# Kernel optimization log

Measured on AMD Instinct MI355X. Metric: run time of the kernel, lower is better.

## Reference

```python
import jax, jax.numpy as jnp
import numpy as np

EPS_NORM = 1e-6
EPS_MM = 1e-5


def feature_l2norm(f, axis=1):
    # torch: f / sqrt(sum(f^2, dim) + 1e-6)
    return f / jnp.sqrt(jnp.sum(f * f, axis=axis, keepdims=True) + EPS_NORM)


def mutual_matching(c):
    # c: [b, 1, f1, f2, f3, f4]
    b, ch, f1, f2, f3, f4 = c.shape
    # max over (f1,f2) for each (f3,f4) target location
    max_B = jnp.max(c.reshape(b, f1 * f2, f3, f4), axis=1).reshape(b, 1, 1, 1, f3, f4)
    # max over (f3,f4) for each (f1,f2) source location
    max_A = jnp.max(c.reshape(b, f1 * f2, f3 * f4), axis=2).reshape(b, 1, f1, f2, 1, 1)
    return c * (c / (max_A + EPS_MM)) * (c / (max_B + EPS_MM))


def correlation4d(fa, fb):
    # fa: [b,c,hA,wA], fb: [b,c,hB,wB] -> [b,1,hA,wA,hB,wB]
    corr = jnp.einsum('bcij,bckl->bijkl', fa, fb)[:, None]
    corr = jax.nn.relu(corr)
    return feature_l2norm(corr, axis=1)  # channel dim is 1 -> x/sqrt(x^2+eps)


def conv4d(x, w, b):
    # x: [B,Ci,f1,f2,f3,f4]; w: [Co,Ci,k,k,k,k]; b: [Co]
    # Implemented as a sum of k 3D convs over (f2,f3,f4), sliding along f1 --
    # exactly the Conv4d emulation used by NC-Net.
    B, Ci, f1, f2, f3, f4 = x.shape
    Co, _, k = w.shape[:3]
    p = k // 2
    xp = jnp.pad(x, ((0, 0), (0, 0), (p, p), (0, 0), (0, 0), (0, 0)))
    out = None
    for i in range(k):
        xi = jax.lax.dynamic_slice_in_dim(xp, i, f1, axis=2)        # [B,Ci,f1,f2,f3,f4]
        xi = xi.transpose(0, 2, 1, 3, 4, 5).reshape(B * f1, Ci, f2, f3, f4)
        yi = jax.lax.conv_general_dilated(
            xi, w[:, :, i], window_strides=(1, 1, 1),
            padding=[(p, p)] * 3,
            dimension_numbers=('NCDHW', 'OIDHW', 'NCDHW'))
        yi = yi.reshape(B, f1, Co, f2, f3, f4).transpose(0, 2, 1, 3, 4, 5)
        out = yi if out is None else out + yi
    return out + b[None, :, None, None, None, None]


def nc_stack(x, params):
    # Sequential(Conv4d, ReLU) x 3
    for w, b in params:
        x = jax.nn.relu(conv4d(x, w, b))
    return x


def neigh_consensus(x, params):
    # symmetric mode: conv(x) + conv(x.permute(0,1,4,5,2,3)).permute back
    ya = nc_stack(x, params)
    yb = nc_stack(x.transpose(0, 1, 4, 5, 2, 3), params).transpose(0, 1, 4, 5, 2, 3)
    return ya + yb


def setup_inputs() -> dict:
    key = jax.random.key(0)
    ks = jax.random.split(key, 8)
    b, c, h, w = 4, 256, 32, 32
    feature_A = jax.random.normal(ks[0], (b, c, h, w), dtype=jnp.float32)
    feature_B = jax.random.normal(ks[1], (b, c, h, w), dtype=jnp.float32)
    k = 3
    w1 = jax.random.normal(ks[2], (10, 1, k, k, k, k), dtype=jnp.float32) * 0.05
    b1 = jnp.zeros((10,), jnp.float32)
    w2 = jax.random.normal(ks[3], (10, 10, k, k, k, k), dtype=jnp.float32) * 0.05
    b2 = jnp.zeros((10,), jnp.float32)
    w3 = jax.random.normal(ks[4], (1, 10, k, k, k, k), dtype=jnp.float32) * 0.05
    b3 = jnp.zeros((1,), jnp.float32)
    return {"feature_A": feature_A, "feature_B": feature_B,
            "w1": w1, "b1": b1, "w2": w2, "b2": b2, "w3": w3, "b3": b3}


def reference(feature_A, feature_B, w1, b1, w2, b2, w3, b3):
    fa = feature_l2norm(feature_A, axis=1)
    fb = feature_l2norm(feature_B, axis=1)
    corr4d = correlation4d(fa, fb)                   # [b,1,hA,wA,hB,wB]
    corr4d = mutual_matching(corr4d)
    corr4d = neigh_consensus(corr4d, [(w1, b1), (w2, b2), (w3, b3)])
    corr4d = mutual_matching(corr4d)
    return corr4d
```

## Files before the change

kernel.cpp:

```cpp
#include <hip/hip_runtime.h>

#define EPSN 1e-6f
#define EPSM 1e-5f

typedef __fp16 h2v __attribute__((ext_vector_type(2)));
typedef __fp16 f16x4 __attribute__((ext_vector_type(4)));
typedef float f32x4 __attribute__((ext_vector_type(4)));

#define MFMA16(a, b, c) __builtin_amdgcn_mfma_f32_16x16x16f16((a), (b), (c), 0, 0, 0)

__device__ __forceinline__ unsigned pkh2(float a, float b) {
    union { h2v h; unsigned u; } v;
    v.h = __builtin_amdgcn_cvt_pkrtz(a, b);
    return v.u;
}

__device__ __forceinline__ float dot2f(unsigned a, unsigned b, float c) {
    union { unsigned u; h2v h; } ua, ub;
    ua.u = a; ub.u = b;
#if __has_builtin(__builtin_amdgcn_fdot2)
    return __builtin_amdgcn_fdot2(ua.h, ub.h, c, false);
#else
    return fmaf((float)ua.h.x, (float)ub.h.x,
                fmaf((float)ua.h.y, (float)ub.h.y, c));
#endif
}

__global__ __launch_bounds__(256) void invnorm_k(const float* __restrict__ f,
                                                 float* __restrict__ inv)
{
    int pbase = blockIdx.x * 64;
    int pp = threadIdx.x & 63;
    int cc = threadIdx.x >> 6;
    int pos = pbase + pp;
    int b = pos >> 10, ij = pos & 1023;
    const float* fp = f + (size_t)(b * 256) * 1024 + ij;
    float s = 0.f;
    #pragma unroll 8
    for (int k = 0; k < 64; ++k) {
        float v = fp[(size_t)(cc * 64 + k) * 1024];
        s += v * v;
    }
    __shared__ float red[4][64];
    red[cc][pp] = s;
    __syncthreads();
    if (cc == 0) {
        float t = red[0][pp] + red[1][pp] + red[2][pp] + red[3][pp];
        inv[pos] = rsqrtf(t + EPSN);
    }
}

__global__ __launch_bounds__(256) void corr_k(const float* __restrict__ fa,
                                              const float* __restrict__ fb,
                                              const float* __restrict__ invA,
                                              const float* __restrict__ invB,
                                              float* __restrict__ corr)
{
    __shared__ float As[16][68];
    __shared__ float Bs[16][68];
    int b = blockIdx.z;
    int i0 = blockIdx.y * 64, j0 = blockIdx.x * 64;
    int tid = threadIdx.x;
    int tx = tid & 15, ty = tid >> 4;
    const float* fab = fa + (size_t)b * 256 * 1024;
    const float* fbb = fb + (size_t)b * 256 * 1024;
    const float* ia = invA + b * 1024 + i0;
    const float* ib = invB + b * 1024 + j0;
    float acc[4][4] = {};
    for (int kc = 0; kc < 256; kc += 16) {
        #pragma unroll
        for (int l = 0; l < 4; ++l) {
            int idx = tid + l * 256;
            int r = idx >> 6, cix = idx & 63;
            As[r][cix] = fab[(size_t)(kc + r) * 1024 + i0 + cix] * ia[cix];
            Bs[r][cix] = fbb[(size_t)(kc + r) * 1024 + j0 + cix] * ib[cix];
        }
        __syncthreads();
        #pragma unroll
        for (int k = 0; k < 16; ++k) {
            float4 av = *(const float4*)&As[k][ty * 4];
            float4 bv = *(const float4*)&Bs[k][tx * 4];
            float a[4] = {av.x, av.y, av.z, av.w};
            float bq[4] = {bv.x, bv.y, bv.z, bv.w};
            #pragma unroll
            for (int ii = 0; ii < 4; ++ii)
                #pragma unroll
                for (int jj = 0; jj < 4; ++jj)
                    acc[ii][jj] += a[ii] * bq[jj];
        }
        __syncthreads();
    }
    float* cb = corr + ((size_t)b << 20);
    #pragma unroll
    for (int ii = 0; ii < 4; ++ii) {
        float4 o; float v;
        v = fmaxf(acc[ii][0], 0.f); o.x = v * rsqrtf(v * v + EPSN);
        v = fmaxf(acc[ii][1], 0.f); o.y = v * rsqrtf(v * v + EPSN);
        v = fmaxf(acc[ii][2], 0.f); o.z = v * rsqrtf(v * v + EPSN);
        v = fmaxf(acc[ii][3], 0.f); o.w = v * rsqrtf(v * v + EPSN);
        *(float4*)&cb[(size_t)(i0 + ty * 4 + ii) * 1024 + j0 + tx * 4] = o;
    }
}

__global__ __launch_bounds__(256) void rowmax_k(const float* __restrict__ c,
                                                float* __restrict__ maxR)
{
    int b = blockIdx.y, i = blockIdx.x, tid = threadIdx.x;
    const float* row = c + ((size_t)b << 20) + ((size_t)i << 10);
    float m = fmaxf(fmaxf(row[tid], row[tid + 256]), fmaxf(row[tid + 512], row[tid + 768]));
    #pragma unroll
    for (int off = 32; off; off >>= 1) m = fmaxf(m, __shfl_down(m, off, 64));
    __shared__ float sred[4];
    if ((tid & 63) == 0) sred[tid >> 6] = m;
    __syncthreads();
    if (tid == 0)
        maxR[b * 1024 + i] = fmaxf(fmaxf(sred[0], sred[1]), fmaxf(sred[2], sred[3]));
}

__global__ __launch_bounds__(256) void colmax_k(const float* __restrict__ c,
                                                float* __restrict__ maxC)
{
    int j = blockIdx.x * 256 + threadIdx.x;
    int r0 = blockIdx.y * 128;
    int b = blockIdx.z;
    const float* cb = c + ((size_t)b << 20);
    float m = 0.f;
    for (int r = 0; r < 128; ++r) m = fmaxf(m, cb[(size_t)(r0 + r) * 1024 + j]);
    atomicMax((int*)&maxC[b * 1024 + j], __float_as_int(m));
}

__global__ __launch_bounds__(256) void mmapply_k(float* __restrict__ c,
                                                 const float* __restrict__ maxR,
                                                 const float* __restrict__ maxC)
{
    int e4 = blockIdx.x * 256 + threadIdx.x;
    int e = e4 * 4;
    int b = e >> 20, i = (e >> 10) & 1023, j0 = e & 1023;
    float4 v = ((float4*)c)[e4];
    float ra = 1.f / (maxR[b * 1024 + i] + EPSM);
    float4 mb = ((const float4*)maxC)[(b * 1024 + j0) >> 2];
    float4 o;
    o.x = v.x * v.x * v.x * ra / (mb.x + EPSM);
    o.y = v.y * v.y * v.y * ra / (mb.y + EPSM);
    o.z = v.z * v.z * v.z * ra / (mb.z + EPSM);
    o.w = v.w * v.w * v.w * ra / (mb.w + EPSM);
    ((float4*)c)[e4] = o;
}

template <int CI, int CO>
__global__ void packw_k(const float* __restrict__ w, float* __restrict__ dst, int perm)
{
    constexpr int WS = (3 * CO + 3) & ~3;
    int idx = blockIdx.x * 256 + threadIdx.x;
    if (idx >= CI * 27 * WS) return;
    int ci = idx / (27 * WS);
    int rem = idx - ci * 27 * WS;
    int d123 = rem / WS;
    int slot = rem - d123 * WS;
    float v = 0.f;
    if (slot < 3 * CO) {
        int d4 = slot / CO, co = slot - d4 * CO;
        int t = d123 * 3 + d4;
        int d1 = t / 27, r2 = t % 27;
        int d2 = r2 / 9, r3 = r2 % 9;
        int d3 = r3 / 3, dd4 = r3 % 3;
        int st = perm ? (d3 * 27 + dd4 * 9 + d1 * 3 + d2) : t;
        v = w[(co * CI + ci) * 81 + st];
    }
    dst[idx] = v;
}

__global__ void packwm_k(const float* __restrict__ w, unsigned short* __restrict__ dst,
                         int perm)
{
    int idx = blockIdx.x * 256 + threadIdx.x;
    if (idx >= 20736) return;
    int tap = idx >> 8;
    int co  = (idx >> 4) & 15;
    int k   = idx & 15;
    float v = 0.f;
    if (co < 10 && k < 10) {
        int d1 = tap / 27, r2 = tap % 27;
        int d2 = r2 / 9, r3 = r2 % 9;
        int d3 = r3 / 3, d4 = r3 % 3;
        int st = perm ? (d3 * 27 + d4 * 9 + d1 * 3 + d2) : tap;
        v = w[(co * 10 + k) * 81 + st];
    }
    union { __fp16 h; unsigned short u; } cv;
    cv.h = (__fp16)v;
    dst[idx] = cv.u;
}

template <int CIP, int CO>
__global__ void packw2_k(const float* __restrict__ w, unsigned* __restrict__ dst, int perm)
{
    constexpr int WS = (3 * CO + 3) & ~3;
    int idx = blockIdx.x * 256 + threadIdx.x;
    if (idx >= CIP * 27 * WS) return;
    int pp = idx / (27 * WS);
    int rem = idx - pp * 27 * WS;
    int d123 = rem / WS;
    int slot = rem - d123 * WS;
    unsigned v = 0u;
    if (slot < 3 * CO) {
        int d4 = slot / CO, co = slot - d4 * CO;
        int t = d123 * 3 + d4;
        int d1 = t / 27, r2 = t % 27;
        int d2 = r2 / 9, r3 = r2 % 9;
        int d3 = r3 / 3, dd4 = r3 % 3;
        int st = perm ? (d3 * 27 + dd4 * 9 + d1 * 3 + d2) : t;
        float f0 = w[(co * 2 * CIP + 2 * pp) * 81 + st];
        float f1 = w[(co * 2 * CIP + 2 * pp + 1) * 81 + st];
        v = pkh2(f0, f1);
    }
    dst[idx] = v;
}

template <int CI, int CO, bool ADD, bool PACK>
__global__ __launch_bounds__(256, 4) void conv4d_k(const float* __restrict__ x,
                                                   const float* __restrict__ wp,
                                                   const float* __restrict__ bias,
                                                   float* __restrict__ y)
{
    constexpr int WS = (3 * CO + 3) & ~3;
    constexpr int NW4 = WS / 4;
    constexpr int SLAB = 34 * 35;
    __shared__ float tile[3 * SLAB];

    int tid = threadIdx.x;
    int f1 = blockIdx.x >> 5, f2 = blockIdx.x & 31;
    int q = tid & 7, yy = tid >> 3;
    int x0 = q << 2;

    for (int e = tid; e < 3 * SLAB; e += 256) tile[e] = 0.f;

    float acc[CO][4];
    #pragma unroll
    for (int co = 0; co < CO; ++co) {
        float bv = bias[co];
        acc[co][0] = bv; acc[co][1] = bv; acc[co][2] = bv; acc[co][3] = bv;
    }

    float bufA[WS], bufB[WS];

#define TAP(U, WB, WN, PF) do {                                               \
        constexpr int u_ = (U);                                               \
        const float* rowb_ = &tile[(u_/3)*SLAB + (yy + u_%3)*35 + x0];        \
        float xs_[6];                                                         \
        _Pragma("unroll") for (int j = 0; j < 6; ++j) xs_[j] = rowb_[j];      \
        if (PF) {                                                             \
            _Pragma("unroll") for (int k = 0; k < NW4; ++k)                   \
                *(float4*)&WN[k*4] =                                          \
                    ((const float4*)(wphase + (u_+1)*WS))[k];                 \
        }                                                                     \
        _Pragma("unroll") for (int d4 = 0; d4 < 3; ++d4)                      \
        _Pragma("unroll") for (int co = 0; co < CO; ++co) {                   \
            float wf_ = WB[d4*CO + co];                                       \
            _Pragma("unroll") for (int p = 0; p < 4; ++p)                     \
                acc[co][p] = fmaf(xs_[p + d4], wf_, acc[co][p]);              \
        }                                                                     \
    } while (0)

    #pragma unroll 1
    for (int ci = 0; ci < CI; ++ci) {
        const float* wci = wp + ci * 27 * WS;
        #pragma unroll 1
        for (int d1 = 0; d1 < 3; ++d1) {
            int g1 = f1 + d1 - 1;
            bool g1ok = (unsigned)g1 < 32u;
            const float* wphase = wci + d1 * 9 * WS;
            __syncthreads();
            #pragma unroll
            for (int k = 0; k < NW4; ++k)
                *(float4*)&bufA[k*4] = ((const float4*)wphase)[k];
            #pragma unroll
            for (int it = 0; it < 3; ++it) {
                int e = tid + it * 256;
                int s2 = e >> 8, rr = (e >> 3) & 31, qq = e & 7;
                int g2 = f2 + s2 - 1;
                float4 v = {0.f, 0.f, 0.f, 0.f};
                if (g1ok & ((unsigned)g2 < 32u))
                    v = *(const float4*)&x[((size_t)ci << 20) +
                        ((size_t)((g1 << 5) + g2) << 10) + (rr << 5) + (qq << 2)];
                float* t = &tile[s2 * SLAB + (rr + 1) * 35 + 1 + (qq << 2)];
                t[0] = v.x; t[1] = v.y; t[2] = v.z; t[3] = v.w;
            }
            __syncthreads();

            TAP(0, bufA, bufB, true);
            TAP(1, bufB, bufA, true);
            TAP(2, bufA, bufB, true);
            TAP(3, bufB, bufA, true);
            TAP(4, bufA, bufB, true);
            TAP(5, bufB, bufA, true);
            TAP(6, bufA, bufB, true);
            TAP(7, bufB, bufA, true);
            TAP(8, bufA, bufB, false);
        }
    }
#undef TAP

    size_t obase = ((size_t)(f1 * 32 + f2) << 10) + yy * 32 + x0;
    if (PACK) {
        unsigned* ypu = (unsigned*)y;
        #pragma unroll
        for (int c = 0; c < CO / 2; ++c) {
            uint4 o;
            o.x = pkh2(fmaxf(acc[2*c][0], 0.f), fmaxf(acc[2*c+1][0], 0.f));
            o.y = pkh2(fmaxf(acc[2*c][1], 0.f), fmaxf(acc[2*c+1][1], 0.f));
            o.z = pkh2(fmaxf(acc[2*c][2], 0.f), fmaxf(acc[2*c+1][2], 0.f));
            o.w = pkh2(fmaxf(acc[2*c][3], 0.f), fmaxf(acc[2*c+1][3], 0.f));
            *(uint4*)&ypu[(size_t)c * 1048576 + obase] = o;
        }
    } else {
        #pragma unroll
        for (int co = 0; co < CO; ++co) {
            float4 o;
            o.x = fmaxf(acc[co][0], 0.f);
            o.y = fmaxf(acc[co][1], 0.f);
            o.z = fmaxf(acc[co][2], 0.f);
            o.w = fmaxf(acc[co][3], 0.f);
            float* yp = y + ((size_t)co << 20) + obase;
            if (ADD) {
                float4 prev = *(const float4*)yp;
                o.x += prev.x; o.y += prev.y; o.z += prev.z; o.w += prev.w;
            }
            *(float4*)yp = o;
        }
    }
}

__global__ __launch_bounds__(256, 4) void conv4dm_k(const unsigned* __restrict__ xp,
                                                    const unsigned short* __restrict__ wm,
                                                    const float* __restrict__ bias,
                                                    unsigned* __restrict__ yp)
{
    __shared__ unsigned tile[3 * 10 * 34 * 9];

    int tid = threadIdx.x;
    int bx = blockIdx.x;
    int chunk  = bx & 7;
    int within = bx >> 3;
    int f1 = (chunk << 2) | (within >> 7);
    int f2 = (within >> 2) & 31;
    int q  = within & 3;

    int l  = tid & 63;
    int wv = tid >> 6;
    int sl = l & 15;
    int g  = l >> 4;

    for (int e = tid; e < 9180; e += 256) tile[e] = 0u;

    f32x4 bv;
    #pragma unroll
    for (int e = 0; e < 4; ++e) {
        int co = 4 * g + e;
        bv[e] = (co < 10) ? bias[co] : 0.f;
    }
    f32x4 acc0 = bv, acc1 = bv, acc2 = bv, acc3 = bv;

    int qbase = q * 8;

    #pragma unroll 1
    for (int d1 = 0; d1 < 3; ++d1) {
        int g1 = f1 + d1 - 1;
        bool g1ok = (unsigned)g1 < 32u;
        __syncthreads();

        uint2 aw[27];
        #pragma unroll
        for (int t27 = 0; t27 < 27; ++t27) {
            int tap = d1 * 27 + t27;
            aw[t27] = *(const uint2*)&wm[(tap << 8) + (sl << 4) + (g << 2)];
        }

        if (tid < 240) {
            int k  = tid & 7;
            int rg = tid >> 3;
            int r  = rg % 10;
            int s2 = rg / 10;
            int c  = 1 + (k << 2);
            int g2 = f2 + s2 - 1;
            int g3 = qbase + r - 1;
            uint4 v0 = {0,0,0,0}, v1 = {0,0,0,0}, v2 = {0,0,0,0},
                  v3 = {0,0,0,0}, v4 = {0,0,0,0};
            if (g1ok & ((unsigned)g2 < 32u) & ((unsigned)g3 < 32u)) {
                size_t off = ((size_t)((g1 << 5) + g2) << 10) + (g3 << 5) + (c - 1);
                v0 = *(const uint4*)&xp[off];
                v1 = *(const uint4*)&xp[off + 1048576];
                v2 = *(const uint4*)&xp[off + 2097152];
                v3 = *(const uint4*)&xp[off + 3145728];
                v4 = *(const uint4*)&xp[off + 4194304];
            }
            unsigned* tb = &tile[((s2 * 10 + r) * 34 + c) * 9];
            tb[0] = v0.x; tb[9]  = v0.y; tb[18] = v0.z; tb[27] = v0.w;
            tb[1] = v1.x; tb[10] = v1.y; tb[19] = v1.z; tb[28] = v1.w;
            tb[2] = v2.x; tb[11] = v2.y; tb[20] = v2.z; tb[29] = v2.w;
            tb[3] = v3.x; tb[12] = v3.y; tb[21] = v3.z; tb[30] = v3.w;
            tb[4] = v4.x; tb[13] = v4.y; tb[22] = v4.z; tb[31] = v4.w;
        }
        __syncthreads();

        int tb0 = ((wv * 2 + 0) * 34 + sl) * 9 + (g << 1);
        #pragma unroll
        for (int d2 = 0; d2 < 3; ++d2)
        #pragma unroll
        for (int d3 = 0; d3 < 3; ++d3)
        #pragma unroll
        for (int d4 = 0; d4 < 3; ++d4) {
            int t27 = d2 * 9 + d3 * 3 + d4;
            union { uint2 u; f16x4 h; } A; A.u = aw[t27];
            int tapoff = ((d2 * 10 + d3) * 34 + d4) * 9;
            const unsigned* bp = &tile[tb0 + tapoff];
            union { uint2 u; f16x4 h; } B;
            B.u.x = bp[0];           B.u.y = bp[1];
            acc0 = MFMA16(A.h, B.h, acc0);
            B.u.x = bp[16 * 9];      B.u.y = bp[16 * 9 + 1];
            acc1 = MFMA16(A.h, B.h, acc1);
            B.u.x = bp[34 * 9];      B.u.y = bp[34 * 9 + 1];
            acc2 = MFMA16(A.h, B.h, acc2);
            B.u.x = bp[50 * 9];      B.u.y = bp[50 * 9 + 1];
            acc3 = MFMA16(A.h, B.h, acc3);
        }
    }

    __syncthreads();
#define EPST(ACC, RT, CH) do {                                                \
        int row_ = (RT);                                                      \
        int col_ = (CH) * 16 + sl;                                            \
        float r0 = fmaxf((ACC)[0], 0.f), r1 = fmaxf((ACC)[1], 0.f);           \
        float r2 = fmaxf((ACC)[2], 0.f), r3 = fmaxf((ACC)[3], 0.f);           \
        if (g < 2) {                                                          \
            tile[((2*g)     * 8 + row_) * 33 + col_] = pkh2(r0, r1);          \
            tile[((2*g + 1) * 8 + row_) * 33 + col_] = pkh2(r2, r3);          \
        } else if (g == 2) {                                                  \
            tile[(4 * 8 + row_) * 33 + col_] = pkh2(r0, r1);                  \
        }                                                                     \
    } while (0)
    EPST(acc0, wv * 2 + 0, 0);
    EPST(acc1, wv * 2 + 0, 1);
    EPST(acc2, wv * 2 + 1, 0);
    EPST(acc3, wv * 2 + 1, 1);
#undef EPST
    __syncthreads();

    size_t pbase = ((size_t)((f1 << 5) + f2) << 10);
    #pragma unroll
    for (int u = tid; u < 320; u += 256) {
        int p   = u >> 6;
        int rem = u & 63;
        int row = rem >> 3;
        int cg  = rem & 7;
        const unsigned* src = &tile[(p * 8 + row) * 33 + (cg << 2)];
        uint4 v;
        v.x = src[0]; v.y = src[1]; v.z = src[2]; v.w = src[3];
        *(uint4*)&yp[(size_t)p * 1048576 + pbase +
                     ((size_t)(qbase + row) << 5) + (cg << 2)] = v;
    }
}

template <int CIP, int CO, bool ADD>
__global__ __launch_bounds__(256, 4) void conv4dp_k(const unsigned* __restrict__ xp,
                                                    const unsigned* __restrict__ wp,
                                                    const float* __restrict__ bias,
                                                    float* __restrict__ y)
{
    constexpr int WS = (3 * CO + 3) & ~3;
    constexpr int NW4 = WS / 4;
    constexpr int SLAB = 34 * 35;
    __shared__ unsigned tile[3 * SLAB];

    int tid = threadIdx.x;
    int f1 = blockIdx.x >> 5, f2 = blockIdx.x & 31;
    int q = tid & 7, yy = tid >> 3;
    int x0 = q << 2;

    for (int e = tid; e < 3 * SLAB; e += 256) tile[e] = 0u;

    float acc[CO][4];
    #pragma unroll
    for (int co = 0; co < CO; ++co) {
        float bvv = bias[co];
        acc[co][0] = bvv; acc[co][1] = bvv; acc[co][2] = bvv; acc[co][3] = bvv;
    }

    unsigned bufA[WS], bufB[WS];

#define TAPP(U, WB, WN, PF) do {                                              \
        constexpr int u_ = (U);                                               \
        const unsigned* rowb_ = &tile[(u_/3)*SLAB + (yy + u_%3)*35 + x0];     \
        unsigned xs_[6];                                                      \
        _Pragma("unroll") for (int j = 0; j < 6; ++j) xs_[j] = rowb_[j];      \
        if (PF) {                                                             \
            _Pragma("unroll") for (int k = 0; k < NW4; ++k)                   \
                *(uint4*)&WN[k*4] =                                           \
                    ((const uint4*)(wphase + (u_+1)*WS))[k];                  \
        }                                                                     \
        _Pragma("unroll") for (int d4 = 0; d4 < 3; ++d4)                      \
        _Pragma("unroll") for (int co = 0; co < CO; ++co) {                   \
            unsigned wf_ = WB[d4*CO + co];                                    \
            _Pragma("unroll") for (int p = 0; p < 4; ++p)                     \
                acc[co][p] = dot2f(xs_[p + d4], wf_, acc[co][p]);             \
        }                                                                     \
    } while (0)

    #pragma unroll 1
    for (int pp = 0; pp < CIP; ++pp) {
        const unsigned* wci = wp + pp * 27 * WS;
        #pragma unroll 1
        for (int d1 = 0; d1 < 3; ++d1) {
            int g1 = f1 + d1 - 1;
            bool g1ok = (unsigned)g1 < 32u;
            const unsigned* wphase = wci + d1 * 9 * WS;
            __syncthreads();
            #pragma unroll
            for (int k = 0; k < NW4; ++k)
                *(uint4*)&bufA[k*4] = ((const uint4*)wphase)[k];
            #pragma unroll
            for (int it = 0; it < 3; ++it) {
                int e = tid + it * 256;
                int s2 = e >> 8, rr = (e >> 3) & 31, qq = e & 7;
                int g2 = f2 + s2 - 1;
                uint4 v = {0u, 0u, 0u, 0u};
                if (g1ok & ((unsigned)g2 < 32u))
                    v = *(const uint4*)&xp[((size_t)pp << 20) +
                        ((size_t)((g1 << 5) + g2) << 10) + (rr << 5) + (qq << 2)];
                unsigned* t = &tile[s2 * SLAB + (rr + 1) * 35 + 1 + (qq << 2)];
                t[0] = v.x; t[1] = v.y; t[2] = v.z; t[3] = v.w;
            }
            __syncthreads();

            TAPP(0, bufA, bufB, true);
            TAPP(1, bufB, bufA, true);
            TAPP(2, bufA, bufB, true);
            TAPP(3, bufB, bufA, true);
            TAPP(4, bufA, bufB, true);
            TAPP(5, bufB, bufA, true);
            TAPP(6, bufA, bufB, true);
            TAPP(7, bufB, bufA, true);
            TAPP(8, bufA, bufB, false);
        }
    }
#undef TAPP

    size_t obase = ((size_t)(f1 * 32 + f2) << 10) + yy * 32 + x0;
    #pragma unroll
    for (int co = 0; co < CO; ++co) {
        float4 o;
        o.x = fmaxf(acc[co][0], 0.f);
        o.y = fmaxf(acc[co][1], 0.f);
        o.z = fmaxf(acc[co][2], 0.f);
        o.w = fmaxf(acc[co][3], 0.f);
        float* ypt = y + ((size_t)co << 20) + obase;
        if (ADD) {
            float4 prev = *(const float4*)ypt;
            o.x += prev.x; o.y += prev.y; o.z += prev.z; o.w += prev.w;
        }
        *(float4*)ypt = o;
    }
}

extern "C" void kernel_launch(void* const* d_in, const int* in_sizes, int n_in,
                              void* d_out, int out_size, void* d_ws, size_t ws_size,
                              hipStream_t stream)
{
    (void)in_sizes; (void)n_in; (void)out_size; (void)ws_size;
    const float* fA = (const float*)d_in[0];
    const float* fB = (const float*)d_in[1];
    const float* w1 = (const float*)d_in[2];
    const float* b1 = (const float*)d_in[3];
    const float* w2 = (const float*)d_in[4];
    const float* b2 = (const float*)d_in[5];
    const float* w3 = (const float*)d_in[6];
    const float* b3 = (const float*)d_in[7];
    float* out = (float*)d_out;
    float* ws = (float*)d_ws;

    size_t o = 0;
    float* invA = ws + o; o += 4096;
    float* invB = ws + o; o += 4096;
    float* maxR = ws + o; o += 4096;
    float* maxC = ws + o; o += 4096;
    float* pw1  = ws + o; o += 2048;
    unsigned short* wm2 = (unsigned short*)(ws + o); o += 20736;
    unsigned* pw3 = (unsigned*)(ws + o); o += 1080;
    float* corr = ws + o; o += 4194304;
    unsigned* t1p = (unsigned*)(ws + o); o += 5242880;
    unsigned* t2p = (unsigned*)(ws + o); o += 5242880;

    invnorm_k<<<64, 256, 0, stream>>>(fA, invA);
    invnorm_k<<<64, 256, 0, stream>>>(fB, invB);
    corr_k<<<dim3(16, 16, 4), 256, 0, stream>>>(fA, fB, invA, invB, corr);

    rowmax_k<<<dim3(1024, 4), 256, 0, stream>>>(corr, maxR);
    (void)hipMemsetAsync(maxC, 0, 4096 * sizeof(float), stream);
    colmax_k<<<dim3(4, 8, 4), 256, 0, stream>>>(corr, maxC);
    mmapply_k<<<4096, 256, 0, stream>>>(corr, maxR, maxC);

    packw_k<1, 10><<<4, 256, 0, stream>>>(w1, pw1, 0);
    packw_k<1, 10><<<4, 256, 0, stream>>>(w1, pw1 + 864, 1);
    packwm_k<<<81, 256, 0, stream>>>(w2, wm2, 0);
    packwm_k<<<81, 256, 0, stream>>>(w2, wm2 + 20736, 1);
    packw2_k<5, 1><<<3, 256, 0, stream>>>(w3, pw3, 0);
    packw2_k<5, 1><<<3, 256, 0, stream>>>(w3, pw3 + 540, 1);

    for (int b = 0; b < 4; ++b) {
        const float* xb = corr + (size_t)b * 1048576;
        float* ob = out + (size_t)b * 1048576;
        conv4d_k<1, 10, false, true><<<1024, 256, 0, stream>>>(xb, pw1, b1, (float*)t1p);
        conv4dm_k<<<4096, 256, 0, stream>>>(t1p, wm2, b2, t2p);
        conv4dp_k<5, 1, false><<<1024, 256, 0, stream>>>(t2p, pw3, b3, ob);
        conv4d_k<1, 10, false, true><<<1024, 256, 0, stream>>>(xb, pw1 + 864, b1, (float*)t1p);
        conv4dm_k<<<4096, 256, 0, stream>>>(t1p, wm2 + 20736, b2, t2p);
        conv4dp_k<5, 1, true ><<<1024, 256, 0, stream>>>(t2p, pw3 + 540, b3, ob);
    }

    rowmax_k<<<dim3(1024, 4), 256, 0, stream>>>(out, maxR);
    (void)hipMemsetAsync(maxC, 0, 4096 * sizeof(float), stream);
    colmax_k<<<dim3(4, 8, 4), 256, 0, stream>>>(out, maxC);
    mmapply_k<<<4096, 256, 0, stream>>>(out, maxR, maxC);
}
```

Baseline: 1.565 ms.

## Prefetch next input slab into registers during compute in conv kernels

Both conv4d kernels now load the next d1 (and next channel-pair) input slab from global memory into registers before the MFMA/dot2 compute of the current slab, then write it to LDS after the next barrier. This software-pipelines global loads against compute so memory latency is hidden instead of exposed between barriers. Index math for staging is hoisted out of the loop, and the MFMA kernel raises wave priority during the compute section. The cost is higher register pressure from the held prefetch values, which may reduce occupancy.

```diff
diff --git a/kernel.cpp b/kernel.cpp
--- a/kernel.cpp
+++ b/kernel.cpp
@@ -362,46 +362,54 @@
 
     int qbase = q * 8;
 
+    bool stager = tid < 240;
+    int sk = tid & 7, srg = tid >> 3;
+    int sr = srg % 10, ss2 = srg / 10;
+    int sc = 1 + (sk << 2);
+    int sg2 = f2 + ss2 - 1;
+    int sg3 = qbase + sr - 1;
+    bool sok = ((unsigned)sg2 < 32u) & ((unsigned)sg3 < 32u);
+    size_t sbase = (((size_t)(unsigned)sg2) << 10) + (sg3 << 5) + (sc - 1);
+    unsigned* stp = &tile[((ss2 * 10 + sr) * 34 + sc) * 9];
+
+    uint4 v0, v1, v2, v3, v4;
+#define LOADP(G1) do {                                                        \
+        if (stager) {                                                         \
+            if (sok & ((unsigned)(G1) < 32u)) {                               \
+                size_t off_ = (((size_t)(unsigned)(G1)) << 15) + sbase;       \
+                v0 = *(const uint4*)&xp[off_];                                \
+                v1 = *(const uint4*)&xp[off_ + 1048576];                      \
+                v2 = *(const uint4*)&xp[off_ + 2097152];                      \
+                v3 = *(const uint4*)&xp[off_ + 3145728];                      \
+                v4 = *(const uint4*)&xp[off_ + 4194304];                      \
+            } else {                                                          \
+                v0 = v1 = v2 = v3 = v4 = (uint4){0u, 0u, 0u, 0u};             \
+            }                                                                 \
+        }                                                                     \
+    } while (0)
+
+    LOADP(f1 - 1);
+
     #pragma unroll 1
     for (int d1 = 0; d1 < 3; ++d1) {
-        int g1 = f1 + d1 - 1;
-        bool g1ok = (unsigned)g1 < 32u;
+        uint2 aw[27];
+        #pragma unroll
+        for (int t27 = 0; t27 < 27; ++t27)
+            aw[t27] = *(const uint2*)&wm[((d1 * 27 + t27) << 8) + (sl << 4) + (g << 2)];
+
         __syncthreads();
-
-        uint2 aw[27];
-        #pragma unroll
-        for (int t27 = 0; t27 < 27; ++t27) {
-            int tap = d1 * 27 + t27;
-            aw[t27] = *(const uint2*)&wm[(tap << 8) + (sl << 4) + (g << 2)];
-        }
-
-        if (tid < 240) {
-            int k  = tid & 7;
-            int rg = tid >> 3;
-            int r  = rg % 10;
-            int s2 = rg / 10;
-            int c  = 1 + (k << 2);
-            int g2 = f2 + s2 - 1;
-            int g3 = qbase + r - 1;
-            uint4 v0 = {0,0,0,0}, v1 = {0,0,0,0}, v2 = {0,0,0,0},
-                  v3 = {0,0,0,0}, v4 = {0,0,0,0};
-            if (g1ok & ((unsigned)g2 < 32u) & ((unsigned)g3 < 32u)) {
-                size_t off = ((size_t)((g1 << 5) + g2) << 10) + (g3 << 5) + (c - 1);
-                v0 = *(const uint4*)&xp[off];
-                v1 = *(const uint4*)&xp[off + 1048576];
-                v2 = *(const uint4*)&xp[off + 2097152];
-                v3 = *(const uint4*)&xp[off + 3145728];
-                v4 = *(const uint4*)&xp[off + 4194304];
-            }
-            unsigned* tb = &tile[((s2 * 10 + r) * 34 + c) * 9];
-            tb[0] = v0.x; tb[9]  = v0.y; tb[18] = v0.z; tb[27] = v0.w;
-            tb[1] = v1.x; tb[10] = v1.y; tb[19] = v1.z; tb[28] = v1.w;
-            tb[2] = v2.x; tb[11] = v2.y; tb[20] = v2.z; tb[29] = v2.w;
-            tb[3] = v3.x; tb[12] = v3.y; tb[21] = v3.z; tb[30] = v3.w;
-            tb[4] = v4.x; tb[13] = v4.y; tb[22] = v4.z; tb[31] = v4.w;
-        }
+        if (stager) {
+            stp[0] = v0.x; stp[9]  = v0.y; stp[18] = v0.z; stp[27] = v0.w;
+            stp[1] = v1.x; stp[10] = v1.y; stp[19] = v1.z; stp[28] = v1.w;
+            stp[2] = v2.x; stp[11] = v2.y; stp[20] = v2.z; stp[29] = v2.w;
+            stp[3] = v3.x; stp[12] = v3.y; stp[21] = v3.z; stp[30] = v3.w;
+            stp[4] = v4.x; stp[13] = v4.y; stp[22] = v4.z; stp[31] = v4.w;
+        }
+        if (d1 < 2)
+            LOADP(f1 + d1);
         __syncthreads();
 
+        __builtin_amdgcn_s_setprio(1);
         int tb0 = ((wv * 2 + 0) * 34 + sl) * 9 + (g << 1);
         #pragma unroll
         for (int d2 = 0; d2 < 3; ++d2)
@@ -423,7 +431,9 @@
             B.u.x = bp[50 * 9];      B.u.y = bp[50 * 9 + 1];
             acc3 = MFMA16(A.h, B.h, acc3);
         }
-    }
+        __builtin_amdgcn_s_setprio(0);
+    }
+#undef LOADP
 
     __syncthreads();
 #define EPST(ACC, RT, CH) do {                                                \
@@ -487,6 +497,32 @@
 
     unsigned bufA[WS], bufB[WS];
 
+    const int e0 = tid, e1 = tid + 256, e2 = tid + 512;
+#define STG(I, EV)                                                            \
+    const int s2_##I = (EV) >> 8, rr_##I = ((EV) >> 3) & 31, qq_##I = (EV) & 7;\
+    const int g2_##I = f2 + s2_##I - 1;                                       \
+    const bool ok_##I = (unsigned)g2_##I < 32u;                               \
+    const size_t so_##I = (((size_t)(unsigned)g2_##I) << 10) +                \
+                          (rr_##I << 5) + (qq_##I << 2);                      \
+    unsigned* tp_##I = &tile[s2_##I * SLAB + (rr_##I + 1) * 35 + 1 + (qq_##I << 2)];
+    STG(0, e0) STG(1, e1) STG(2, e2)
+#undef STG
+
+    uint4 sv0, sv1, sv2;
+#define ISSUE(PPN, G1N) do {                                                  \
+        bool g1k_ = (unsigned)(G1N) < 32u;                                    \
+        const unsigned* xb_ = xp + ((size_t)(PPN) << 20) +                    \
+                              (((size_t)(unsigned)(G1N)) << 15);              \
+        if (g1k_ & ok_0) sv0 = *(const uint4*)&xb_[so_0];                     \
+        else             sv0 = (uint4){0u, 0u, 0u, 0u};                       \
+        if (g1k_ & ok_1) sv1 = *(const uint4*)&xb_[so_1];                     \
+        else             sv1 = (uint4){0u, 0u, 0u, 0u};                       \
+        if (g1k_ & ok_2) sv2 = *(const uint4*)&xb_[so_2];                     \
+        else             sv2 = (uint4){0u, 0u, 0u, 0u};                       \
+    } while (0)
+
+    ISSUE(0, f1 - 1);
+
 #define TAPP(U, WB, WN, PF) do {                                              \
         constexpr int u_ = (U);                                               \
         const unsigned* rowb_ = &tile[(u_/3)*SLAB + (yy + u_%3)*35 + x0];     \
@@ -510,25 +546,18 @@
         const unsigned* wci = wp + pp * 27 * WS;
         #pragma unroll 1
         for (int d1 = 0; d1 < 3; ++d1) {
-            int g1 = f1 + d1 - 1;
-            bool g1ok = (unsigned)g1 < 32u;
             const unsigned* wphase = wci + d1 * 9 * WS;
             __syncthreads();
+            tp_0[0] = sv0.x; tp_0[1] = sv0.y; tp_0[2] = sv0.z; tp_0[3] = sv0.w;
+            tp_1[0] = sv1.x; tp_1[1] = sv1.y; tp_1[2] = sv1.z; tp_1[3] = sv1.w;
+            tp_2[0] = sv2.x; tp_2[1] = sv2.y; tp_2[2] = sv2.z; tp_2[3] = sv2.w;
+            int d1n = d1 + 1, ppn = pp;
+            if (d1n == 3) { d1n = 0; ppn = pp + 1; }
+            if (ppn < CIP)
+                ISSUE(ppn, f1 + d1n - 1);
             #pragma unroll
             for (int k = 0; k < NW4; ++k)
                 *(uint4*)&bufA[k*4] = ((const uint4*)wphase)[k];
-            #pragma unroll
-            for (int it = 0; it < 3; ++it) {
-                int e = tid + it * 256;
-                int s2 = e >> 8, rr = (e >> 3) & 31, qq = e & 7;
-                int g2 = f2 + s2 - 1;
-                uint4 v = {0u, 0u, 0u, 0u};
-                if (g1ok & ((unsigned)g2 < 32u))
-                    v = *(const uint4*)&xp[((size_t)pp << 20) +
-                        ((size_t)((g1 << 5) + g2) << 10) + (rr << 5) + (qq << 2)];
-                unsigned* t = &tile[s2 * SLAB + (rr + 1) * 35 + 1 + (qq << 2)];
-                t[0] = v.x; t[1] = v.y; t[2] = v.z; t[3] = v.w;
-            }
             __syncthreads();
 
             TAPP(0, bufA, bufB, true);
@@ -543,6 +572,7 @@
         }
     }
 #undef TAPP
+#undef ISSUE
 
     size_t obase = ((size_t)(f1 * 32 + f2) << 10) + yy * 32 + x0;
     #pragma unroll
```

New measurement: 1.783 ms. +13.9%, slower.

## Batch symmetric conv branches via grid.y, reuse LDS operands in MFMA conv, fuse final conv

Applied to the files above, without the earlier changes.

Both symmetric branches of the first two conv4d layers now run in one launch each, with grid.y selecting the branch's weights and intermediate buffers, which doubles the workspace for the intermediates. The MFMA conv2 kernel remaps each wave to a 4-row by 16-column tile and loads six B fragments once per (d2,d4), reusing them across the three d3 taps to cut LDS reads; it also hoists the weight loads above the barrier and raises wave priority during compute. The final conv3 is specialised into one kernel that processes both branches and sums their ReLU outputs directly, removing the separate read-add-write launch. The result is fewer launches and less redundant memory traffic, at the cost of larger intermediate buffers and higher register pressure in the conv2 kernel.

```diff
diff --git a/kernel.cpp b/kernel.cpp
--- a/kernel.cpp
+++ b/kernel.cpp
@@ -216,7 +216,7 @@
     dst[idx] = v;
 }
 
-template <int CI, int CO, bool ADD, bool PACK>
+template <int CI, int CO>
 __global__ __launch_bounds__(256, 4) void conv4d_k(const float* __restrict__ x,
                                                    const float* __restrict__ wp,
                                                    const float* __restrict__ bias,
@@ -231,6 +231,8 @@
     int f1 = blockIdx.x >> 5, f2 = blockIdx.x & 31;
     int q = tid & 7, yy = tid >> 3;
     int x0 = q << 2;
+    const float* wpb = wp + blockIdx.y * (CI * 27 * WS);
+    unsigned* ypu = (unsigned*)y + (size_t)blockIdx.y * 5242880;
 
     for (int e = tid; e < 3 * SLAB; e += 256) tile[e] = 0.f;
 
@@ -263,7 +265,7 @@
 
     #pragma unroll 1
     for (int ci = 0; ci < CI; ++ci) {
-        const float* wci = wp + ci * 27 * WS;
+        const float* wci = wpb + ci * 27 * WS;
         #pragma unroll 1
         for (int d1 = 0; d1 < 3; ++d1) {
             int g1 = f1 + d1 - 1;
@@ -301,32 +303,14 @@
 #undef TAP
 
     size_t obase = ((size_t)(f1 * 32 + f2) << 10) + yy * 32 + x0;
-    if (PACK) {
-        unsigned* ypu = (unsigned*)y;
-        #pragma unroll
-        for (int c = 0; c < CO / 2; ++c) {
-            uint4 o;
-            o.x = pkh2(fmaxf(acc[2*c][0], 0.f), fmaxf(acc[2*c+1][0], 0.f));
-            o.y = pkh2(fmaxf(acc[2*c][1], 0.f), fmaxf(acc[2*c+1][1], 0.f));
-            o.z = pkh2(fmaxf(acc[2*c][2], 0.f), fmaxf(acc[2*c+1][2], 0.f));
-            o.w = pkh2(fmaxf(acc[2*c][3], 0.f), fmaxf(acc[2*c+1][3], 0.f));
-            *(uint4*)&ypu[(size_t)c * 1048576 + obase] = o;
-        }
-    } else {
-        #pragma unroll
-        for (int co = 0; co < CO; ++co) {
-            float4 o;
-            o.x = fmaxf(acc[co][0], 0.f);
-            o.y = fmaxf(acc[co][1], 0.f);
-            o.z = fmaxf(acc[co][2], 0.f);
-            o.w = fmaxf(acc[co][3], 0.f);
-            float* yp = y + ((size_t)co << 20) + obase;
-            if (ADD) {
-                float4 prev = *(const float4*)yp;
-                o.x += prev.x; o.y += prev.y; o.z += prev.z; o.w += prev.w;
-            }
-            *(float4*)yp = o;
-        }
+    #pragma unroll
+    for (int c = 0; c < CO / 2; ++c) {
+        uint4 o;
+        o.x = pkh2(fmaxf(acc[2*c][0], 0.f), fmaxf(acc[2*c+1][0], 0.f));
+        o.y = pkh2(fmaxf(acc[2*c][1], 0.f), fmaxf(acc[2*c+1][1], 0.f));
+        o.z = pkh2(fmaxf(acc[2*c][2], 0.f), fmaxf(acc[2*c+1][2], 0.f));
+        o.w = pkh2(fmaxf(acc[2*c][3], 0.f), fmaxf(acc[2*c+1][3], 0.f));
+        *(uint4*)&ypu[(size_t)c * 1048576 + obase] = o;
     }
 }
 
@@ -345,10 +329,16 @@
     int f2 = (within >> 2) & 31;
     int q  = within & 3;
 
+    const unsigned* xpb = xp + (size_t)blockIdx.y * 5242880;
+    const unsigned short* wmb = wm + blockIdx.y * 20736;
+    unsigned* ypb = yp + (size_t)blockIdx.y * 5242880;
+
     int l  = tid & 63;
     int wv = tid >> 6;
     int sl = l & 15;
     int g  = l >> 4;
+    int rt = (wv & 1) << 2;
+    int ch = wv >> 1;
 
     for (int e = tid; e < 9180; e += 256) tile[e] = 0u;
 
@@ -358,7 +348,7 @@
         int co = 4 * g + e;
         bv[e] = (co < 10) ? bias[co] : 0.f;
     }
-    f32x4 acc0 = bv, acc1 = bv, acc2 = bv, acc3 = bv;
+    f32x4 accv[4] = {bv, bv, bv, bv};
 
     int qbase = q * 8;
 
@@ -366,34 +356,31 @@
     for (int d1 = 0; d1 < 3; ++d1) {
         int g1 = f1 + d1 - 1;
         bool g1ok = (unsigned)g1 < 32u;
-        __syncthreads();
 
         uint2 aw[27];
         #pragma unroll
-        for (int t27 = 0; t27 < 27; ++t27) {
-            int tap = d1 * 27 + t27;
-            aw[t27] = *(const uint2*)&wm[(tap << 8) + (sl << 4) + (g << 2)];
-        }
+        for (int t27 = 0; t27 < 27; ++t27)
+            aw[t27] = *(const uint2*)&wmb[((d1 * 27 + t27) << 8) + (sl << 4) + (g << 2)];
+
+        __syncthreads();
 
         if (tid < 240) {
-            int k  = tid & 7;
-            int rg = tid >> 3;
-            int r  = rg % 10;
-            int s2 = rg / 10;
-            int c  = 1 + (k << 2);
-            int g2 = f2 + s2 - 1;
-            int g3 = qbase + r - 1;
+            int sk = tid & 7, srg = tid >> 3;
+            int sr = srg % 10, ss2 = srg / 10;
+            int sc = 1 + (sk << 2);
+            int g2 = f2 + ss2 - 1;
+            int g3 = qbase + sr - 1;
             uint4 v0 = {0,0,0,0}, v1 = {0,0,0,0}, v2 = {0,0,0,0},
                   v3 = {0,0,0,0}, v4 = {0,0,0,0};
             if (g1ok & ((unsigned)g2 < 32u) & ((unsigned)g3 < 32u)) {
-                size_t off = ((size_t)((g1 << 5) + g2) << 10) + (g3 << 5) + (c - 1);
-                v0 = *(const uint4*)&xp[off];
-                v1 = *(const uint4*)&xp[off + 1048576];
-                v2 = *(const uint4*)&xp[off + 2097152];
-                v3 = *(const uint4*)&xp[off + 3145728];
-                v4 = *(const uint4*)&xp[off + 4194304];
+                size_t off = ((size_t)((g1 << 5) + g2) << 10) + (g3 << 5) + (sc - 1);
+                v0 = *(const uint4*)&xpb[off];
+                v1 = *(const uint4*)&xpb[off + 1048576];
+                v2 = *(const uint4*)&xpb[off + 2097152];
+                v3 = *(const uint4*)&xpb[off + 3145728];
+                v4 = *(const uint4*)&xpb[off + 4194304];
             }
-            unsigned* tb = &tile[((s2 * 10 + r) * 34 + c) * 9];
+            unsigned* tb = &tile[((ss2 * 10 + sr) * 34 + sc) * 9];
             tb[0] = v0.x; tb[9]  = v0.y; tb[18] = v0.z; tb[27] = v0.w;
             tb[1] = v1.x; tb[10] = v1.y; tb[19] = v1.z; tb[28] = v1.w;
             tb[2] = v2.x; tb[11] = v2.y; tb[20] = v2.z; tb[29] = v2.w;
@@ -402,27 +389,30 @@
         }
         __syncthreads();
 
-        int tb0 = ((wv * 2 + 0) * 34 + sl) * 9 + (g << 1);
+        __builtin_amdgcn_s_setprio(1);
         #pragma unroll
         for (int d2 = 0; d2 < 3; ++d2)
         #pragma unroll
-        for (int d3 = 0; d3 < 3; ++d3)
-        #pragma unroll
         for (int d4 = 0; d4 < 3; ++d4) {
-            int t27 = d2 * 9 + d3 * 3 + d4;
-            union { uint2 u; f16x4 h; } A; A.u = aw[t27];
-            int tapoff = ((d2 * 10 + d3) * 34 + d4) * 9;
-            const unsigned* bp = &tile[tb0 + tapoff];
-            union { uint2 u; f16x4 h; } B;
-            B.u.x = bp[0];           B.u.y = bp[1];
-            acc0 = MFMA16(A.h, B.h, acc0);
-            B.u.x = bp[16 * 9];      B.u.y = bp[16 * 9 + 1];
-            acc1 = MFMA16(A.h, B.h, acc1);
-            B.u.x = bp[34 * 9];      B.u.y = bp[34 * 9 + 1];
-            acc2 = MFMA16(A.h, B.h, acc2);
-            B.u.x = bp[50 * 9];      B.u.y = bp[50 * 9 + 1];
-            acc3 = MFMA16(A.h, B.h, acc3);
+            unsigned b0[6], b1[6];
+            #pragma unroll
+            for (int j = 0; j < 6; ++j) {
+                int idx = ((d2 * 10 + rt + j) * 34 + ch * 16 + sl + d4) * 9 + (g << 1);
+                b0[j] = tile[idx];
+                b1[j] = tile[idx + 1];
+            }
+            #pragma unroll
+            for (int d3 = 0; d3 < 3; ++d3) {
+                union { uint2 u; f16x4 h; } A; A.u = aw[d2 * 9 + d3 * 3 + d4];
+                #pragma unroll
+                for (int j2 = 0; j2 < 4; ++j2) {
+                    union { uint2 u; f16x4 h; } B;
+                    B.u.x = b0[j2 + d3]; B.u.y = b1[j2 + d3];
+                    accv[j2] = MFMA16(A.h, B.h, accv[j2]);
+                }
+            }
         }
+        __builtin_amdgcn_s_setprio(0);
     }
 
     __syncthreads();
@@ -438,10 +428,10 @@
             tile[(4 * 8 + row_) * 33 + col_] = pkh2(r0, r1);                  \
         }                                                                     \
     } while (0)
-    EPST(acc0, wv * 2 + 0, 0);
-    EPST(acc1, wv * 2 + 0, 1);
-    EPST(acc2, wv * 2 + 1, 0);
-    EPST(acc3, wv * 2 + 1, 1);
+    EPST(accv[0], rt + 0, ch);
+    EPST(accv[1], rt + 1, ch);
+    EPST(accv[2], rt + 2, ch);
+    EPST(accv[3], rt + 3, ch);
 #undef EPST
     __syncthreads();
 
@@ -455,19 +445,16 @@
         const unsigned* src = &tile[(p * 8 + row) * 33 + (cg << 2)];
         uint4 v;
         v.x = src[0]; v.y = src[1]; v.z = src[2]; v.w = src[3];
-        *(uint4*)&yp[(size_t)p * 1048576 + pbase +
-                     ((size_t)(qbase + row) << 5) + (cg << 2)] = v;
-    }
-}
-
-template <int CIP, int CO, bool ADD>
-__global__ __launch_bounds__(256, 4) void conv4dp_k(const unsigned* __restrict__ xp,
-                                                    const unsigned* __restrict__ wp,
-                                                    const float* __restrict__ bias,
-                                                    float* __restrict__ y)
-{
-    constexpr int WS = (3 * CO + 3) & ~3;
-    constexpr int NW4 = WS / 4;
+        *(uint4*)&ypb[(size_t)p * 1048576 + pbase +
+                      ((size_t)(qbase + row) << 5) + (cg << 2)] = v;
+    }
+}
+
+__global__ __launch_bounds__(256, 4) void conv4dpf_k(const unsigned* __restrict__ xp,
+                                                     const unsigned* __restrict__ wp,
+                                                     const float* __restrict__ bias,
+                                                     float* __restrict__ y)
+{
     constexpr int SLAB = 34 * 35;
     __shared__ unsigned tile[3 * SLAB];
 
@@ -478,87 +465,59 @@
 
     for (int e = tid; e < 3 * SLAB; e += 256) tile[e] = 0u;
 
-    float acc[CO][4];
-    #pragma unroll
-    for (int co = 0; co < CO; ++co) {
-        float bvv = bias[co];
-        acc[co][0] = bvv; acc[co][1] = bvv; acc[co][2] = bvv; acc[co][3] = bvv;
-    }
-
-    unsigned bufA[WS], bufB[WS];
-
-#define TAPP(U, WB, WN, PF) do {                                              \
-        constexpr int u_ = (U);                                               \
-        const unsigned* rowb_ = &tile[(u_/3)*SLAB + (yy + u_%3)*35 + x0];     \
-        unsigned xs_[6];                                                      \
-        _Pragma("unroll") for (int j = 0; j < 6; ++j) xs_[j] = rowb_[j];      \
-        if (PF) {                                                             \
-            _Pragma("unroll") for (int k = 0; k < NW4; ++k)                   \
-                *(uint4*)&WN[k*4] =                                           \
-                    ((const uint4*)(wphase + (u_+1)*WS))[k];                  \
-        }                                                                     \
-        _Pragma("unroll") for (int d4 = 0; d4 < 3; ++d4)                      \
-        _Pragma("unroll") for (int co = 0; co < CO; ++co) {                   \
-            unsigned wf_ = WB[d4*CO + co];                                    \
-            _Pragma("unroll") for (int p = 0; p < 4; ++p)                     \
-                acc[co][p] = dot2f(xs_[p + d4], wf_, acc[co][p]);             \
-        }                                                                     \
-    } while (0)
+    float bv = bias[0];
+    float res0 = 0.f, res1 = 0.f, res2 = 0.f, res3 = 0.f;
 
     #pragma unroll 1
-    for (int pp = 0; pp < CIP; ++pp) {
-        const unsigned* wci = wp + pp * 27 * WS;
+    for (int half = 0; half < 2; ++half) {
+        const unsigned* xph = xp + ((size_t)half * 5242880);
+        const unsigned* wph = wp + half * 540;
+        float a0 = bv, a1 = bv, a2 = bv, a3 = bv;
         #pragma unroll 1
-        for (int d1 = 0; d1 < 3; ++d1) {
-            int g1 = f1 + d1 - 1;
-            bool g1ok = (unsigned)g1 < 32u;
-            const unsigned* wphase = wci + d1 * 9 * WS;
-            __syncthreads();
-            #pragma unroll
-            for (int k = 0; k < NW4; ++k)
-                *(uint4*)&bufA[k*4] = ((const uint4*)wphase)[k];
-            #pragma unroll
-            for (int it = 0; it < 3; ++it) {
-                int e = tid + it * 256;
-                int s2 = e >> 8, rr = (e >> 3) & 31, qq = e & 7;
-                int g2 = f2 + s2 - 1;
-                uint4 v = {0u, 0u, 0u, 0u};
-                if (g1ok & ((unsigned)g2 < 32u))
-                    v = *(const uint4*)&xp[((size_t)pp << 20) +
-                        ((size_t)((g1 << 5) + g2) << 10) + (rr << 5) + (qq << 2)];
-                unsigned* t = &tile[s2 * SLAB + (rr + 1) * 35 + 1 + (qq << 2)];
-                t[0] = v.x; t[1] = v.y; t[2] = v.z; t[3] = v.w;
+        for (int pp = 0; pp < 5; ++pp) {
+            const unsigned* wci = wph + pp * 108;
+            #pragma unroll 1
+            for (int d1 = 0; d1 < 3; ++d1) {
+                int g1 = f1 + d1 - 1;
+                bool g1ok = (unsigned)g1 < 32u;
+                const unsigned* wphase = wci + d1 * 36;
+                __syncthreads();
+                #pragma unroll
+                for (int it = 0; it < 3; ++it) {
+                    int e = tid + it * 256;
+                    int s2 = e >> 8, rr = (e >> 3) & 31, qq = e & 7;
+                    int g2 = f2 + s2 - 1;
+                    uint4 v = {0u, 0u, 0u, 0u};
+                    if (g1ok & ((unsigned)g2 < 32u))
+                        v = *(const uint4*)&xph[((size_t)pp << 20) +
+                            ((size_t)((g1 << 5) + g2) << 10) + (rr << 5) + (qq << 2)];
+                    unsigned* t = &tile[s2 * SLAB + (rr + 1) * 35 + 1 + (qq << 2)];
+                    t[0] = v.x; t[1] = v.y; t[2] = v.z; t[3] = v.w;
+                }
+                __syncthreads();
+
+                #pragma unroll
+                for (int u = 0; u < 9; ++u) {
+                    const unsigned* rowb = &tile[(u / 3) * SLAB + (yy + u % 3) * 35 + x0];
+                    unsigned xs0 = rowb[0], xs1 = rowb[1], xs2 = rowb[2];
+                    unsigned xs3 = rowb[3], xs4 = rowb[4], xs5 = rowb[5];
+                    uint4 wt = *(const uint4*)&wphase[u * 4];
+                    a0 = dot2f(xs0, wt.x, a0); a1 = dot2f(xs1, wt.x, a1);
+                    a2 = dot2f(xs2, wt.x, a2); a3 = dot2f(xs3, wt.x, a3);
+                    a0 = dot2f(xs1, wt.y, a0); a1 = dot2f(xs2, wt.y, a1);
+                    a2 = dot2f(xs3, wt.y, a2); a3 = dot2f(xs4, wt.y, a3);
+                    a0 = dot2f(xs2, wt.z, a0); a1 = dot2f(xs3, wt.z, a1);
+                    a2 = dot2f(xs4, wt.z, a2); a3 = dot2f(xs5, wt.z, a3);
+                }
             }
-            __syncthreads();
-
-            TAPP(0, bufA, bufB, true);
-            TAPP(1, bufB, bufA, true);
-            TAPP(2, bufA, bufB, true);
-            TAPP(3, bufB, bufA, true);
-            TAPP(4, bufA, bufB, true);
-            TAPP(5, bufB, bufA, true);
-            TAPP(6, bufA, bufB, true);
-            TAPP(7, bufB, bufA, true);
-            TAPP(8, bufA, bufB, false);
         }
-    }
-#undef TAPP
+        res0 += fmaxf(a0, 0.f); res1 += fmaxf(a1, 0.f);
+        res2 += fmaxf(a2, 0.f); res3 += fmaxf(a3, 0.f);
+    }
 
     size_t obase = ((size_t)(f1 * 32 + f2) << 10) + yy * 32 + x0;
-    #pragma unroll
-    for (int co = 0; co < CO; ++co) {
-        float4 o;
-        o.x = fmaxf(acc[co][0], 0.f);
-        o.y = fmaxf(acc[co][1], 0.f);
-        o.z = fmaxf(acc[co][2], 0.f);
-        o.w = fmaxf(acc[co][3], 0.f);
-        float* ypt = y + ((size_t)co << 20) + obase;
-        if (ADD) {
-            float4 prev = *(const float4*)ypt;
-            o.x += prev.x; o.y += prev.y; o.z += prev.z; o.w += prev.w;
-        }
-        *(float4*)ypt = o;
-    }
+    float4 o = {res0, res1, res2, res3};
+    *(float4*)&y[obase] = o;
 }
 
 extern "C" void kernel_launch(void* const* d_in, const int* in_sizes, int n_in,
@@ -586,8 +545,8 @@
     unsigned short* wm2 = (unsigned short*)(ws + o); o += 20736;
     unsigned* pw3 = (unsigned*)(ws + o); o += 1080;
     float* corr = ws + o; o += 4194304;
-    unsigned* t1p = (unsigned*)(ws + o); o += 5242880;
-    unsigned* t2p = (unsigned*)(ws + o); o += 5242880;
+    unsigned* t1p = (unsigned*)(ws + o); o += 10485760;
+    unsigned* t2p = (unsigned*)(ws + o); o += 10485760;
 
     invnorm_k<<<64, 256, 0, stream>>>(fA, invA);
     invnorm_k<<<64, 256, 0, stream>>>(fB, invB);
@@ -608,12 +567,9 @@
     for (int b = 0; b < 4; ++b) {
         const float* xb = corr + (size_t)b * 1048576;
         float* ob = out + (size_t)b * 1048576;
-        conv4d_k<1, 10, false, true><<<1024, 256, 0, stream>>>(xb, pw1, b1, (float*)t1p);
-        conv4dm_k<<<4096, 256, 0, stream>>>(t1p, wm2, b2, t2p);
-        conv4dp_k<5, 1, false><<<1024, 256, 0, stream>>>(t2p, pw3, b3, ob);
-        conv4d_k<1, 10, false, true><<<1024, 256, 0, stream>>>(xb, pw1 + 864, b1, (float*)t1p);
-        conv4dm_k<<<4096, 256, 0, stream>>>(t1p, wm2 + 20736, b2, t2p);
-        conv4dp_k<5, 1, true ><<<1024, 256, 0, stream>>>(t2p, pw3 + 540, b3, ob);
+        conv4d_k<1, 10><<<dim3(1024, 2), 256, 0, stream>>>(xb, pw1, b1, (float*)t1p);
+        conv4dm_k<<<dim3(4096, 2), 256, 0, stream>>>(t1p, wm2, b2, t2p);
+        conv4dpf_k<<<1024, 256, 0, stream>>>(t2p, pw3, b3, ob);
     }
 
     rowmax_k<<<dim3(1024, 4), 256, 0, stream>>>(out, maxR);
```

New measurement: 2.415 ms. 1.54x slower.
